# Optimization experiments

Hardware: AMD Instinct MI355X
Metric: run time of the kernel (lower is better)

Reference implementation:

```python
import jax, jax.numpy as jnp
import numpy as np

B, T, D = 1, 2048, 2048
HQ, HKV = 32, 8
DKV = 512  # HKV * head_dim

def setup_inputs() -> dict:
    key = jax.random.key(0)
    ks = jax.random.split(key, 5)
    s = 0.02
    return {
        "x": jax.random.normal(ks[0], (B, T, D), jnp.float32),
        "q_proj": jax.random.normal(ks[1], (D, D), jnp.float32) * s,
        "k_proj": jax.random.normal(ks[2], (DKV, D), jnp.float32) * s,
        "v_proj": jax.random.normal(ks[3], (DKV, D), jnp.float32) * s,
        "o_proj": jax.random.normal(ks[4], (D, D), jnp.float32) * s,
    }

def reference(x, q_proj, k_proj, v_proj, o_proj):
    b, t, _ = x.shape
    h_q, h_kv = HQ, HKV
    q_out = x @ q_proj.T            # [b,t,D]
    k_out = x @ k_proj.T            # [b,t,DKV]
    v_out = x @ v_proj.T
    dh_q = q_out.shape[-1] // h_q   # 64
    dh_k = k_out.shape[-1] // h_kv  # 64
    q = q_out.reshape(b, t, h_q, dh_q).transpose(0, 2, 1, 3)   # [b,hq,t,dh]
    k = k_out.reshape(b, t, h_kv, dh_k).transpose(0, 2, 1, 3)  # [b,hkv,t,dh]
    v = v_out.reshape(b, t, h_kv, dh_k).transpose(0, 2, 1, 3)
    group = h_q // h_kv
    k = jnp.repeat(k, group, axis=1)  # [b,hq,t,dh]
    v = jnp.repeat(v, group, axis=1)
    attn_logits = jnp.einsum('bhqd,bhkd->bhqk', q, k) / jnp.sqrt(jnp.float32(dh_q))
    mask = jnp.tril(jnp.ones((t, t), dtype=bool))
    attn = jax.nn.softmax(jnp.where(mask, attn_logits, -1e10), axis=-1)
    ctx = jnp.einsum('bhqk,bhkd->bhqd', attn, v)
    ctx = ctx.transpose(0, 2, 1, 3).reshape(b, t, o_proj.shape[0])
    return ctx @ o_proj
```

## Files before the change

kernel.cpp:

```cpp
#include <hip/hip_runtime.h>
#include <stdint.h>

typedef __attribute__((ext_vector_type(8))) __bf16 bf16x8;
typedef __attribute__((ext_vector_type(8))) unsigned short u16x8;
typedef __attribute__((ext_vector_type(4))) float f32x4;
typedef __attribute__((ext_vector_type(4))) unsigned short u16x4;

typedef __attribute__((address_space(1))) unsigned int as1_uint;
typedef __attribute__((address_space(3))) unsigned int as3_uint;

__device__ __forceinline__ unsigned short f2bf(float f) {
  unsigned int u = __float_as_uint(f);
  u += 0x7fffu + ((u >> 16) & 1u);
  return (unsigned short)(u >> 16);
}

__device__ __forceinline__ void gload_lds16(const void* g, void* l) {
  __builtin_amdgcn_global_load_lds((as1_uint*)(uintptr_t)g, (as3_uint*)(uintptr_t)l,
                                   16, 0, 0);
}

__global__ __launch_bounds__(256)
void cvt_fused(const float* __restrict__ x, const float* __restrict__ qp,
               const float* __restrict__ kp, const float* __restrict__ vp,
               const float* __restrict__ op,
               unsigned short* __restrict__ xb, unsigned short* __restrict__ qpb,
               unsigned short* __restrict__ kpb, unsigned short* __restrict__ vpb,
               unsigned short* __restrict__ opT) {
  __shared__ unsigned short t[64][72];
  const int b = blockIdx.x;
  if (b < 10240) {
    const float* in;
    unsigned short* out;
    int base;
    if (b < 4096)      { in = x;  out = xb;  base = b; }
    else if (b < 8192) { in = qp; out = qpb; base = b - 4096; }
    else if (b < 9216) { in = kp; out = kpb; base = b - 8192; }
    else               { in = vp; out = vpb; base = b - 9216; }
    const int i = base * 256 + threadIdx.x;
    float4 v = ((const float4*)in)[i];
    u16x4 o;
    o[0] = f2bf(v.x); o[1] = f2bf(v.y); o[2] = f2bf(v.z); o[3] = f2bf(v.w);
    ((u16x4*)out)[i] = o;
    return;
  }
  const int tb = b - 10240;
  const int tj = (tb & 31) * 64;
  const int ti = (tb >> 5) * 64;
  const int r  = threadIdx.x >> 4;
  const int c4 = (threadIdx.x & 15) * 4;
#pragma unroll
  for (int i = 0; i < 4; ++i) {
    int row = r + i * 16;
    float4 v = *(const float4*)&op[(size_t)(ti + row) * 2048 + tj + c4];
    t[row][c4]     = f2bf(v.x);
    t[row][c4 + 1] = f2bf(v.y);
    t[row][c4 + 2] = f2bf(v.z);
    t[row][c4 + 3] = f2bf(v.w);
  }
  __syncthreads();
#pragma unroll
  for (int i = 0; i < 4; ++i) {
    int orow = r + i * 16;
    u16x4 o;
    o[0] = t[c4][orow]; o[1] = t[c4 + 1][orow];
    o[2] = t[c4 + 2][orow]; o[3] = t[c4 + 3][orow];
    *(u16x4*)&opT[(size_t)(tj + orow) * 2048 + ti + c4] = o;
  }
}

template <int BN, bool OUT_BF16>
__device__ __forceinline__
void gemm_body(const unsigned short* __restrict__ A,
               const unsigned short* __restrict__ B,
               void* __restrict__ Cout, int N, int K, float alpha,
               int bx, int by, unsigned short* lA, unsigned short* lB) {
  constexpr int NF  = BN / 32;
  constexpr int ASZ = 64 * 64;
  constexpr int BSZ = BN * 64;
  const int tid  = threadIdx.x;
  const int lane = tid & 63;
  const int w    = tid >> 6;
  const int wr   = (w >> 1) * 32;
  const int wc   = (w & 1) * (BN / 2);
  const long brow = (long)by * 64;
  const long bcol = (long)bx * BN;
  const int lr = lane & 15;
  const int lq = lane >> 4;

  const int row0 = tid >> 3;
  const int lc0  = (tid & 7) ^ (row0 & 7);

  f32x4 acc[2][NF] = {};

  const unsigned short* gA = A + (brow + row0) * (long)K + lc0 * 8;
  const unsigned short* gB = B + (bcol + row0) * (long)K + lc0 * 8;

#define G_STAGE(buf, k0)                                                          \
  {                                                                               \
    gload_lds16(gA + (k0),           lA + (buf) * ASZ + tid * 8);                 \
    gload_lds16(gA + 32l * K + (k0), lA + (buf) * ASZ + 2048 + tid * 8);          \
    _Pragma("unroll")                                                             \
    for (int g = 0; g < NF; ++g)                                                  \
      gload_lds16(gB + g * 32l * K + (k0), lB + (buf) * BSZ + g * 2048 + tid * 8);\
  }

  G_STAGE(0, 0);
  __syncthreads();

  for (int k0 = 0; k0 < K; k0 += 64) {
    const int cur = (k0 >> 6) & 1;
    if (k0 + 64 < K) G_STAGE(cur ^ 1, k0 + 64);
#pragma unroll
    for (int kk = 0; kk < 2; ++kk) {
      const int j = kk * 4 + lq;
      const int ra0 = wr + lr, ra1 = wr + 16 + lr;
      bf16x8 a0 = *(const bf16x8*)&lA[cur * ASZ + ra0 * 64 + ((j ^ (ra0 & 7)) << 3)];
      bf16x8 a1 = *(const bf16x8*)&lA[cur * ASZ + ra1 * 64 + ((j ^ (ra1 & 7)) << 3)];
      bf16x8 b[NF];
#pragma unroll
      for (int n = 0; n < NF; ++n) {
        const int rb = wc + n * 16 + lr;
        b[n] = *(const bf16x8*)&lB[cur * BSZ + rb * 64 + ((j ^ (rb & 7)) << 3)];
      }
#pragma unroll
      for (int n = 0; n < NF; ++n) {
        acc[0][n] = __builtin_amdgcn_mfma_f32_16x16x32_bf16(a0, b[n], acc[0][n], 0, 0, 0);
        acc[1][n] = __builtin_amdgcn_mfma_f32_16x16x32_bf16(a1, b[n], acc[1][n], 0, 0, 0);
      }
    }
    __syncthreads();
  }
#undef G_STAGE

  const int orow = (int)brow + wr + lq * 4;
  const int ocol = (int)bcol + wc + lr;
#pragma unroll
  for (int m = 0; m < 2; ++m)
#pragma unroll
    for (int n = 0; n < NF; ++n)
#pragma unroll
      for (int r = 0; r < 4; ++r) {
        size_t row = (size_t)(orow + m * 16 + r);
        size_t col = (size_t)(ocol + n * 16);
        float v = acc[m][n][r] * alpha;
        if (OUT_BF16)
          ((unsigned short*)Cout)[row * N + col] = f2bf(v);
        else
          ((float*)Cout)[row * N + col] = v;
      }
}

template <int BN, bool OUT_BF16>
__global__ __launch_bounds__(256)
void gemm_nt(const unsigned short* __restrict__ A,
             const unsigned short* __restrict__ B,
             void* __restrict__ Cout, int N, int K, float alpha) {
  __shared__ unsigned short lA[2 * 64 * 64];
  __shared__ unsigned short lB[2 * BN * 64];
  const int flat  = (int)blockIdx.x + (int)gridDim.x * (int)blockIdx.y;
  const int total = (int)(gridDim.x * gridDim.y);
  const int cpx   = total >> 3;
  const int swz   = (flat & 7) * cpx + (flat >> 3);
  const int bx    = swz % (int)gridDim.x;
  const int by    = swz / (int)gridDim.x;
  gemm_body<BN, OUT_BF16>(A, B, Cout, N, K, alpha, bx, by, lA, lB);
}

__global__ __launch_bounds__(256)
void gemm_proj(const unsigned short* __restrict__ xb,
               const unsigned short* __restrict__ qpb,
               const unsigned short* __restrict__ kpb,
               const unsigned short* __restrict__ vpb,
               unsigned short* __restrict__ Qb, unsigned short* __restrict__ Kbf,
               unsigned short* __restrict__ Vtb) {
  __shared__ unsigned short lA[2 * 64 * 64];
  __shared__ unsigned short lB[2 * 128 * 64];
  const int raw = blockIdx.x;
  const int bid = (raw & 7) * 96 + (raw >> 3);
  const unsigned short *A, *B;
  unsigned short* C;
  int N, bx, by;
  float alpha;
  if (bid < 512) {
    A = xb;  B = qpb; C = Qb;  N = 2048; alpha = 0.125f * 1.44269504088896f;
    bx = bid & 15; by = bid >> 4;
  } else if (bid < 640) {
    int b = bid - 512;
    A = xb;  B = kpb; C = Kbf; N = 512;  alpha = 1.0f;
    bx = b & 3; by = b >> 2;
  } else {
    int b = bid - 640;
    A = vpb; B = xb;  C = Vtb; N = 2048; alpha = 1.0f;
    bx = b & 15; by = b >> 4;
  }
  gemm_body<128, true>(A, B, C, N, 2048, alpha, bx, by, lA, lB);
}

__global__ __launch_bounds__(256, 4)
void attn64(const unsigned short* __restrict__ Q,
            const unsigned short* __restrict__ Kb,
            const unsigned short* __restrict__ Vt,
            unsigned short* __restrict__ ctx) {
  constexpr int T = 2048, DQ = 2048, DKV = 512, DH = 64;
  const int h    = blockIdx.x;
  const int hkv  = h >> 2;
  const int ya   = blockIdx.y >> 3;
  const int yb   = blockIdx.y & 7;
  const int qi   = (ya == 0) ? yb : (ya == 1) ? 15 - yb : (ya == 2) ? 16 + yb : 31 - yb;
  const int tid  = threadIdx.x;
  const int lane = tid & 63;
  const int lr   = lane & 15;
  const int lq   = lane >> 4;
  const int lk   = lq * 8;
  const int sw   = lr & 7;

  __shared__ unsigned short lK[2][64 * 64];
  __shared__ unsigned short lV[2][64 * 64];

  const int row0 = tid >> 3;
  const int lc0  = (tid & 7) ^ (row0 & 7);
  const int kperm = 8 * ((row0 >> 2) & 3) + 4 * ((row0 >> 4) & 1) + (row0 & 3);

#define STAGE_KV(bufidx, kv0)                                                        \
  {                                                                                  \
    gload_lds16(Kb + (size_t)((kv0) + kperm) * DKV + hkv * DH + lc0 * 8,             \
                &lK[bufidx][tid * 8]);                                               \
    gload_lds16(Kb + (size_t)((kv0) + kperm + 32) * DKV + hkv * DH + lc0 * 8,        \
                &lK[bufidx][2048 + tid * 8]);                                        \
    gload_lds16(Vt + (size_t)(hkv * DH + row0) * T + (kv0) + lc0 * 8,                \
                &lV[bufidx][tid * 8]);                                               \
    gload_lds16(Vt + (size_t)(hkv * DH + row0 + 32) * T + (kv0) + lc0 * 8,           \
                &lV[bufidx][2048 + tid * 8]);                                        \
  }

  const int q0b = qi * 64;
  const int qw  = q0b + (tid >> 6) * 16;

  bf16x8 qf0 = *(const bf16x8*)&Q[(size_t)(qw + lr) * DQ + h * DH + lk];
  bf16x8 qf1 = *(const bf16x8*)&Q[(size_t)(qw + lr) * DQ + h * DH + 32 + lk];

  f32x4 oacc[4] = {};
  float l  = 0.f;
  float mr = -3.0e38f;

  const int nt = qi + 1;
  STAGE_KV(0, 0);
  __syncthreads();

  for (int t = 0; t < nt; ++t) {
    const int kv0 = t * 64;
    const int cur = t & 1;
    if (t + 1 < nt) STAGE_KV(cur ^ 1, kv0 + 64);

    f32x4 s[4];
    __builtin_amdgcn_s_setprio(1);
#pragma unroll
    for (int n = 0; n < 4; ++n) {
      const int krow = n * 16 + lr;
      bf16x8 kf0 = *(const bf16x8*)&lK[cur][krow * 64 + ((lq ^ sw) << 3)];
      bf16x8 kf1 = *(const bf16x8*)&lK[cur][krow * 64 + (((4 + lq) ^ sw) << 3)];
      f32x4 acc = {};
      acc = __builtin_amdgcn_mfma_f32_16x16x32_bf16(kf0, qf0, acc, 0, 0, 0);
      acc = __builtin_amdgcn_mfma_f32_16x16x32_bf16(kf1, qf1, acc, 0, 0, 0);
      s[n] = acc;
    }
    __builtin_amdgcn_s_setprio(0);

    if (t == qi) {
      const int kb = kv0 + 8 * lq;
      const int qg = qw + lr;
#pragma unroll
      for (int n = 0; n < 4; ++n) {
        const int kn = kb + 32 * (n >> 1) + 4 * (n & 1);
#pragma unroll
        for (int r = 0; r < 4; ++r)
          if (kn + r > qg) s[n][r] = -3.0e38f;
      }
    }

    float lml = fmaxf(fmaxf(fmaxf(s[0][0], s[0][1]), fmaxf(s[0][2], s[0][3])),
                      fmaxf(fmaxf(s[1][0], s[1][1]), fmaxf(s[1][2], s[1][3])));
    lml = fmaxf(lml, fmaxf(fmaxf(s[2][0], s[2][1]), fmaxf(s[2][2], s[2][3])));
    lml = fmaxf(lml, fmaxf(fmaxf(s[3][0], s[3][1]), fmaxf(s[3][2], s[3][3])));
    const bool defer = __all(lml <= mr + 8.f);
    if (!defer) {
      float rm = lml;
      rm = fmaxf(rm, __shfl_xor(rm, 16));
      rm = fmaxf(rm, __shfl_xor(rm, 32));
      float mnew = fmaxf(mr, rm);
      float sc   = __builtin_amdgcn_exp2f(mr - mnew);
      mr = mnew;
      l *= sc;
      float sc4[4];
#pragma unroll
      for (int r = 0; r < 4; ++r) sc4[r] = __shfl(sc, (lq << 2) + r);
#pragma unroll
      for (int m = 0; m < 4; ++m)
#pragma unroll
        for (int r = 0; r < 4; ++r) oacc[m][r] *= sc4[r];
    }

    u16x8 pk0, pk1;
    float ps = 0.f;
#pragma unroll
    for (int n = 0; n < 4; ++n)
#pragma unroll
      for (int r = 0; r < 4; ++r) {
        float p = __builtin_amdgcn_exp2f(s[n][r] - mr);
        unsigned int u = __float_as_uint(p);
        ps += __uint_as_float(u & 0xFFFF0000u);
        const int j = ((n & 1) << 2) + r;
        if (n < 2) pk0[j] = (unsigned short)(u >> 16);
        else       pk1[j] = (unsigned short)(u >> 16);
      }
    ps += __shfl_xor(ps, 16);
    ps += __shfl_xor(ps, 32);
    l += ps;
    bf16x8 pf0 = *(bf16x8*)&pk0;
    bf16x8 pf1 = *(bf16x8*)&pk1;

    __builtin_amdgcn_s_setprio(1);
#pragma unroll
    for (int ks = 0; ks < 2; ++ks) {
      bf16x8 pf = ks ? pf1 : pf0;
#pragma unroll
      for (int m = 0; m < 4; ++m) {
        const int vrow = m * 16 + lr;
        bf16x8 vf = *(const bf16x8*)&lV[cur][vrow * 64 + (((ks * 4 + lq) ^ sw) << 3)];
        oacc[m] = __builtin_amdgcn_mfma_f32_16x16x32_bf16(pf, vf, oacc[m], 0, 0, 0);
      }
    }
    __builtin_amdgcn_s_setprio(0);

    __syncthreads();
  }

  float inv[4];
#pragma unroll
  for (int r = 0; r < 4; ++r)
    inv[r] = 1.f / __shfl(l, (lq << 2) + r);
#pragma unroll
  for (int m = 0; m < 4; ++m)
#pragma unroll
    for (int r = 0; r < 4; ++r) {
      int qrow = qw + (lq << 2) + r;
      ctx[(size_t)qrow * DQ + h * DH + m * 16 + lr] = f2bf(oacc[m][r] * inv[r]);
    }
#undef STAGE_KV
}

extern "C" void kernel_launch(void* const* d_in, const int* in_sizes, int n_in,
                              void* d_out, int out_size, void* d_ws, size_t ws_size,
                              hipStream_t stream) {
  const float* x  = (const float*)d_in[0];
  const float* qp = (const float*)d_in[1];
  const float* kp = (const float*)d_in[2];
  const float* vp = (const float*)d_in[3];
  const float* op = (const float*)d_in[4];

  char* ws = (char*)d_ws;
  const size_t MB = 1024 * 1024;
  unsigned short* xb   = (unsigned short*)(ws + 0 * MB);
  unsigned short* qpb  = (unsigned short*)(ws + 8 * MB);
  unsigned short* kpb  = (unsigned short*)(ws + 16 * MB);
  unsigned short* vpb  = (unsigned short*)(ws + 18 * MB);
  unsigned short* opT  = (unsigned short*)(ws + 20 * MB);
  unsigned short* Qb   = (unsigned short*)(ws + 28 * MB);
  unsigned short* Kbf  = (unsigned short*)(ws + 36 * MB);
  unsigned short* Vtb  = (unsigned short*)(ws + 38 * MB);
  unsigned short* ctxb = (unsigned short*)(ws + 40 * MB);

  cvt_fused<<<11264, 256, 0, stream>>>(x, qp, kp, vp, op, xb, qpb, kpb, vpb, opT);

  gemm_proj<<<768, 256, 0, stream>>>(xb, qpb, kpb, vpb, Qb, Kbf, Vtb);

  attn64<<<dim3(32, 32), 256, 0, stream>>>(Qb, Kbf, Vtb, ctxb);

  gemm_nt<128, false><<<dim3(16, 32), 256, 0, stream>>>(ctxb, opT, d_out, 2048, 2048, 1.0f);
}
```

Baseline: 110.8 us.

## Software-pipeline PV MFMA one tile behind QK in causal attention

The P·V matrix multiply for KV tile t-1 is deferred into iteration t, issued right after the Q·K^T MFMAs, with a drain step after the loop. The aim is to let the softmax exp/max work of one tile overlap with MFMA work from another, rather than running them back to back. V staging moves to a triple-buffered LDS ring so the deferred tile's V stays resident while the next one loads. The cost is extra LDS (a third V buffer), more live registers for the carried P fragments, and more complex buffer-index bookkeeping.

```diff
diff --git a/kernel.cpp b/kernel.cpp
--- a/kernel.cpp
+++ b/kernel.cpp
@@ -216,18 +216,21 @@
   const int sw   = lr & 7;
 
   __shared__ unsigned short lK[2][64 * 64];
-  __shared__ unsigned short lV[2][64 * 64];
+  __shared__ unsigned short lV[3][64 * 64];
 
   const int row0 = tid >> 3;
   const int lc0  = (tid & 7) ^ (row0 & 7);
   const int kperm = 8 * ((row0 >> 2) & 3) + 4 * ((row0 >> 4) & 1) + (row0 & 3);
 
-#define STAGE_KV(bufidx, kv0)                                                        \
+#define STAGE_K(bufidx, kv0)                                                         \
   {                                                                                  \
     gload_lds16(Kb + (size_t)((kv0) + kperm) * DKV + hkv * DH + lc0 * 8,             \
                 &lK[bufidx][tid * 8]);                                               \
     gload_lds16(Kb + (size_t)((kv0) + kperm + 32) * DKV + hkv * DH + lc0 * 8,        \
                 &lK[bufidx][2048 + tid * 8]);                                        \
+  }
+#define STAGE_V(bufidx, kv0)                                                         \
+  {                                                                                  \
     gload_lds16(Vt + (size_t)(hkv * DH + row0) * T + (kv0) + lc0 * 8,                \
                 &lV[bufidx][tid * 8]);                                               \
     gload_lds16(Vt + (size_t)(hkv * DH + row0 + 32) * T + (kv0) + lc0 * 8,           \
@@ -243,27 +246,47 @@
   f32x4 oacc[4] = {};
   float l  = 0.f;
   float mr = -3.0e38f;
+  u16x8 pk0p = {}, pk1p = {};
 
   const int nt = qi + 1;
-  STAGE_KV(0, 0);
+  STAGE_K(0, 0);
+  STAGE_V(0, 0);
   __syncthreads();
+
+  int vw = 1;
+  int vr = 2;
 
   for (int t = 0; t < nt; ++t) {
     const int kv0 = t * 64;
-    const int cur = t & 1;
-    if (t + 1 < nt) STAGE_KV(cur ^ 1, kv0 + 64);
+    const int kcur = t & 1;
+    if (t + 1 < nt) {
+      STAGE_K(kcur ^ 1, kv0 + 64);
+      STAGE_V(vw, kv0 + 64);
+    }
 
     f32x4 s[4];
     __builtin_amdgcn_s_setprio(1);
 #pragma unroll
     for (int n = 0; n < 4; ++n) {
       const int krow = n * 16 + lr;
-      bf16x8 kf0 = *(const bf16x8*)&lK[cur][krow * 64 + ((lq ^ sw) << 3)];
-      bf16x8 kf1 = *(const bf16x8*)&lK[cur][krow * 64 + (((4 + lq) ^ sw) << 3)];
+      bf16x8 kf0 = *(const bf16x8*)&lK[kcur][krow * 64 + ((lq ^ sw) << 3)];
+      bf16x8 kf1 = *(const bf16x8*)&lK[kcur][krow * 64 + (((4 + lq) ^ sw) << 3)];
       f32x4 acc = {};
       acc = __builtin_amdgcn_mfma_f32_16x16x32_bf16(kf0, qf0, acc, 0, 0, 0);
       acc = __builtin_amdgcn_mfma_f32_16x16x32_bf16(kf1, qf1, acc, 0, 0, 0);
       s[n] = acc;
+    }
+    if (t > 0) {
+      bf16x8 pf0 = *(bf16x8*)&pk0p;
+      bf16x8 pf1 = *(bf16x8*)&pk1p;
+#pragma unroll
+      for (int m = 0; m < 4; ++m) {
+        const int vrow = m * 16 + lr;
+        bf16x8 vf0 = *(const bf16x8*)&lV[vr][vrow * 64 + ((lq ^ sw) << 3)];
+        bf16x8 vf1 = *(const bf16x8*)&lV[vr][vrow * 64 + (((4 + lq) ^ sw) << 3)];
+        oacc[m] = __builtin_amdgcn_mfma_f32_16x16x32_bf16(pf0, vf0, oacc[m], 0, 0, 0);
+        oacc[m] = __builtin_amdgcn_mfma_f32_16x16x32_bf16(pf1, vf1, oacc[m], 0, 0, 0);
+      }
     }
     __builtin_amdgcn_s_setprio(0);
 
@@ -301,7 +324,6 @@
         for (int r = 0; r < 4; ++r) oacc[m][r] *= sc4[r];
     }
 
-    u16x8 pk0, pk1;
     float ps = 0.f;
 #pragma unroll
     for (int n = 0; n < 4; ++n)
@@ -311,29 +333,29 @@
         unsigned int u = __float_as_uint(p);
         ps += __uint_as_float(u & 0xFFFF0000u);
         const int j = ((n & 1) << 2) + r;
-        if (n < 2) pk0[j] = (unsigned short)(u >> 16);
-        else       pk1[j] = (unsigned short)(u >> 16);
+        if (n < 2) pk0p[j] = (unsigned short)(u >> 16);
+        else       pk1p[j] = (unsigned short)(u >> 16);
       }
     ps += __shfl_xor(ps, 16);
     ps += __shfl_xor(ps, 32);
     l += ps;
-    bf16x8 pf0 = *(bf16x8*)&pk0;
-    bf16x8 pf1 = *(bf16x8*)&pk1;
-
-    __builtin_amdgcn_s_setprio(1);
-#pragma unroll
-    for (int ks = 0; ks < 2; ++ks) {
-      bf16x8 pf = ks ? pf1 : pf0;
-#pragma unroll
-      for (int m = 0; m < 4; ++m) {
-        const int vrow = m * 16 + lr;
-        bf16x8 vf = *(const bf16x8*)&lV[cur][vrow * 64 + (((ks * 4 + lq) ^ sw) << 3)];
-        oacc[m] = __builtin_amdgcn_mfma_f32_16x16x32_bf16(pf, vf, oacc[m], 0, 0, 0);
-      }
-    }
-    __builtin_amdgcn_s_setprio(0);
 
     __syncthreads();
+    vr = vw == 0 ? 2 : vw - 1;
+    vw = vw == 2 ? 0 : vw + 1;
+  }
+
+  {
+    bf16x8 pf0 = *(bf16x8*)&pk0p;
+    bf16x8 pf1 = *(bf16x8*)&pk1p;
+#pragma unroll
+    for (int m = 0; m < 4; ++m) {
+      const int vrow = m * 16 + lr;
+      bf16x8 vf0 = *(const bf16x8*)&lV[vr][vrow * 64 + ((lq ^ sw) << 3)];
+      bf16x8 vf1 = *(const bf16x8*)&lV[vr][vrow * 64 + (((4 + lq) ^ sw) << 3)];
+      oacc[m] = __builtin_amdgcn_mfma_f32_16x16x32_bf16(pf0, vf0, oacc[m], 0, 0, 0);
+      oacc[m] = __builtin_amdgcn_mfma_f32_16x16x32_bf16(pf1, vf1, oacc[m], 0, 0, 0);
+    }
   }
 
   float inv[4];
@@ -347,7 +369,8 @@
       int qrow = qw + (lq << 2) + r;
       ctx[(size_t)qrow * DQ + h * DH + m * 16 + lr] = f2bf(oacc[m][r] * inv[r]);
     }
-#undef STAGE_KV
+#undef STAGE_K
+#undef STAGE_V
 }
 
 extern "C" void kernel_launch(void* const* d_in, const int* in_sizes, int n_in,
```

Result: no change. 111.5 us (+0.7%).
